# Performance work log

Measured on AMD Instinct MI355X. Metric: run time of the kernel, lower is better.

Reference implementation:

```python
import jax, jax.numpy as jnp
import numpy as np

B, N, DIM = 8, 1024, 1024
H, DH = 16, 64           # heads, dim_head; inner_dim = H*DH = 1024
SCALE = DH ** -0.5


def setup_inputs() -> dict:
    key = jax.random.key(0)
    k_x, k_qkv, k_out, k_b = jax.random.split(key, 4)
    inner = H * DH
    x = jax.random.normal(k_x, (B, N, DIM), dtype=jnp.float32)
    # nn.Linear(dim, inner*3, bias=False): y = x @ W_qkv
    W_qkv = jax.random.normal(k_qkv, (DIM, 3 * inner), dtype=jnp.float32) * (DIM ** -0.5)
    # nn.Linear(inner, dim) with bias (project_out is True since heads!=1)
    W_out = jax.random.normal(k_out, (inner, DIM), dtype=jnp.float32) * (inner ** -0.5)
    b_out = jax.random.normal(k_b, (DIM,), dtype=jnp.float32) * 0.01
    return {"x": x, "W_qkv": W_qkv, "W_out": W_out, "b_out": b_out}


def reference(x, W_qkv, W_out, b_out):
    # 'trans' branch of Attention.forward (dropout p=0 -> identity)
    qkv = x @ W_qkv                                   # [b, n, 3*inner]
    q, k, v = jnp.split(qkv, 3, axis=-1)              # each [b, n, inner]
    def to_heads(t):
        b, n, _ = t.shape
        return t.reshape(b, n, H, DH).transpose(0, 2, 1, 3)  # [b, h, n, d]
    q, k, v = to_heads(q), to_heads(k), to_heads(v)
    dots = jnp.einsum('bhid,bhjd->bhij', q, k) * SCALE  # [b, h, n, n]
    attn = jax.nn.softmax(dots, axis=-1)
    out = jnp.einsum('bhij,bhjd->bhid', attn, v)        # [b, h, n, d]
    # original sets attn = out (b h n d) before merging heads
    attn_ret = out
    out_m = out.transpose(0, 2, 1, 3).reshape(B, N, H * DH)  # [b, n, inner]
    proj = out_m @ W_out + b_out                        # [b, n, dim]
    return (proj, attn_ret)
```

## Files before the change

kernel.cpp:

```cpp
#include <hip/hip_runtime.h>
#include <hip/hip_bf16.h>
#include <math.h>

typedef __bf16 bf16_t;
typedef __bf16 bf16x8 __attribute__((ext_vector_type(8)));
typedef __bf16 bf16x4 __attribute__((ext_vector_type(4)));
typedef float f32x4 __attribute__((ext_vector_type(4)));

#define MFMA16(a, b, c) __builtin_amdgcn_mfma_f32_16x16x32_bf16((a), (b), (c), 0, 0, 0)

#define AS3(p) ((__attribute__((address_space(3))) void*)(p))
#define AS1(p) ((const __attribute__((address_space(1))) void*)(p))

#define B_ 8
#define N_ 1024
#define DIM_ 1024
#define H_ 16
#define DH_ 64

#define QSCALE 0.18033688011112042f
#define SM_SHIFT 12.0f

__global__ __launch_bounds__(256) void k_convert(const float* __restrict__ in,
                                                 bf16_t* __restrict__ out) {
    size_t idx = (size_t)blockIdx.x * 256 + threadIdx.x;
    f32x4 v = *(const f32x4*)(in + idx * 4);
    bf16x4 o;
    o[0] = (bf16_t)v[0]; o[1] = (bf16_t)v[1]; o[2] = (bf16_t)v[2]; o[3] = (bf16_t)v[3];
    *(bf16x4*)(out + idx * 4) = o;
}

__global__ __launch_bounds__(256) void k_transpose(const float* __restrict__ in,
                                                   bf16_t* __restrict__ out,
                                                   int R, int C) {
    __shared__ float tile[32][33];
    int c0 = blockIdx.x * 32, r0 = blockIdx.y * 32;
    int tx = threadIdx.x, ty = threadIdx.y;
#pragma unroll
    for (int i = 0; i < 4; ++i)
        tile[ty + 8 * i][tx] = in[(size_t)(r0 + ty + 8 * i) * C + (c0 + tx)];
    __syncthreads();
#pragma unroll
    for (int i = 0; i < 4; ++i)
        out[(size_t)(c0 + ty + 8 * i) * R + (r0 + tx)] = (bf16_t)tile[tx][ty + 8 * i];
}

__global__ __launch_bounds__(256, 2) void k_gemm_qkv(const bf16_t* __restrict__ A,
                                                     const bf16_t* __restrict__ Bt,
                                                     bf16_t* __restrict__ qb,
                                                     bf16_t* __restrict__ kbuf,
                                                     bf16_t* __restrict__ vtb) {
    __shared__ __align__(16) bf16_t As[256 * 64];
    __shared__ __align__(16) bf16_t Bs[128 * 64];
    int tid = threadIdx.x;
    int lane = tid & 63, wave = tid >> 6;
    int quad = lane >> 4, l16 = lane & 15;
    int m0 = blockIdx.y * 256, c0 = blockIdx.x * 128;
    int wm = (wave & 1) * 128, wn = (wave >> 1) * 64;

    const f32x4 vzero = {0.f, 0.f, 0.f, 0.f};
    f32x4 acc[8][4];
#pragma unroll
    for (int i = 0; i < 8; ++i)
#pragma unroll
        for (int j = 0; j < 4; ++j) acc[i][j] = vzero;

    for (int k0 = 0; k0 < 1024; k0 += 64) {
#pragma unroll
        for (int i = 0; i < 8; ++i) {
            int cid = tid + 256 * i;
            int row = cid >> 3;
            int g = (cid & 7) ^ (row & 7);
            __builtin_amdgcn_global_load_lds(
                AS1(A + (size_t)(m0 + row) * 1024 + k0 + g * 8), AS3(As + cid * 8), 16, 0, 0);
        }
#pragma unroll
        for (int i = 0; i < 4; ++i) {
            int cid = tid + 256 * i;
            int row = cid >> 3;
            int g = (cid & 7) ^ (row & 7);
            __builtin_amdgcn_global_load_lds(
                AS1(Bt + (size_t)(c0 + row) * 1024 + k0 + g * 8), AS3(Bs + cid * 8), 16, 0, 0);
        }
        __syncthreads();
#pragma unroll
        for (int c = 0; c < 2; ++c) {
            int s = (4 * c + quad) ^ (l16 & 7);
            bf16x8 bfr[4];
#pragma unroll
            for (int j = 0; j < 4; ++j)
                bfr[j] = *(const bf16x8*)(Bs + (wn + 16 * j + l16) * 64 + s * 8);
#pragma unroll
            for (int i = 0; i < 8; ++i) {
                bf16x8 af = *(const bf16x8*)(As + (wm + 16 * i + l16) * 64 + s * 8);
#pragma unroll
                for (int j = 0; j < 4; ++j)
                    acc[i][j] = MFMA16(af, bfr[j], acc[i][j]);
            }
        }
        __syncthreads();
    }

    int tsel = c0 >> 10;
#pragma unroll
    for (int i = 0; i < 8; ++i) {
#pragma unroll
        for (int r = 0; r < 4; ++r) {
            int m = m0 + wm + 16 * i + quad * 4 + r;
            int b = m >> 10, n = m & 1023;
#pragma unroll
            for (int j = 0; j < 4; ++j) {
                int cc = c0 + wn + 16 * j + l16;
                int ic = cc & 1023;
                int h = ic >> 6, d = ic & 63;
                float val = acc[i][j][r];
                if (tsel == 0)
                    qb[(((size_t)b * H_ + h) * N_ + n) * DH_ + d] = (bf16_t)(val * QSCALE);
                else if (tsel == 1)
                    kbuf[(((size_t)b * H_ + h) * N_ + n) * DH_ + d] = (bf16_t)val;
                else
                    vtb[(((size_t)b * H_ + h) * DH_ + d) * N_ + n] = (bf16_t)val;
            }
        }
    }
}

__global__ __launch_bounds__(256, 2) void k_attn(const bf16_t* __restrict__ q,
                                                 const bf16_t* __restrict__ k,
                                                 const bf16_t* __restrict__ vt,
                                                 float* __restrict__ oattn,
                                                 bf16_t* __restrict__ outm) {
    __shared__ __align__(16) bf16_t KV[2 * 64 * 72];
    __shared__ __align__(16) bf16_t Ps[4 * 4 * 16 * 72];
    bf16_t* Ks = KV;
    bf16_t* Vs = KV + 64 * 72;
    int tid = threadIdx.x;
    int lane = tid & 63, wave = tid >> 6;
    int quad = lane >> 4, l16 = lane & 15;
    int qt = blockIdx.x & 3;
    int bh = blockIdx.x >> 2;
    int b = bh >> 4, h = bh & 15;

    const bf16_t* qp = q + ((size_t)bh * N_ + qt * 256 + wave * 64) * DH_;
    bf16x8 qa[4][2];
#pragma unroll
    for (int g = 0; g < 4; ++g)
#pragma unroll
        for (int c = 0; c < 2; ++c)
            qa[g][c] = *(const bf16x8*)(qp + (size_t)(g * 16 + l16) * DH_ + c * 32 + quad * 8);

    const bf16_t* kp = k + (size_t)bh * N_ * DH_;
    const bf16_t* vp = vt + (size_t)bh * DH_ * N_;
    bf16_t* Pw = Ps + wave * (4 * 16 * 72);

    const f32x4 vzero = {0.f, 0.f, 0.f, 0.f};
    f32x4 o[4][4];
#pragma unroll
    for (int g = 0; g < 4; ++g)
#pragma unroll
        for (int t = 0; t < 4; ++t) o[g][t] = vzero;
    float lsum[4] = {0.f, 0.f, 0.f, 0.f};

    for (int kb = 0; kb < 16; ++kb) {
#pragma unroll
        for (int i = 0; i < 2; ++i) {
            int cid = tid + 256 * i;
            int row = cid >> 3, ch = (cid & 7) * 8;
            *(bf16x8*)(Ks + row * 72 + ch) =
                *(const bf16x8*)(kp + (size_t)(kb * 64 + row) * DH_ + ch);
            *(bf16x8*)(Vs + row * 72 + ch) =
                *(const bf16x8*)(vp + (size_t)row * N_ + kb * 64 + ch);
        }
        __syncthreads();

        f32x4 st[4][4];
#pragma unroll
        for (int jt = 0; jt < 4; ++jt) {
#pragma unroll
            for (int g = 0; g < 4; ++g) st[g][jt] = vzero;
#pragma unroll
            for (int c = 0; c < 2; ++c) {
                bf16x8 kf = *(const bf16x8*)(Ks + (16 * jt + l16) * 72 + c * 32 + quad * 8);
#pragma unroll
                for (int g = 0; g < 4; ++g)
                    st[g][jt] = MFMA16(kf, qa[g][c], st[g][jt]);
            }
        }

#pragma unroll
        for (int g = 0; g < 4; ++g) {
            float ps = 0.f;
#pragma unroll
            for (int jt = 0; jt < 4; ++jt) {
                bf16x4 pk;
#pragma unroll
                for (int r = 0; r < 4; ++r) {
                    float p = __builtin_amdgcn_exp2f(st[g][jt][r] - SM_SHIFT);
                    ps += p;
                    pk[r] = (bf16_t)p;
                }
                *(bf16x4*)(Pw + g * (16 * 72) + l16 * 72 + jt * 16 + quad * 4) = pk;
            }
            lsum[g] += ps;
        }

        bf16x8 pf[4][2];
#pragma unroll
        for (int g = 0; g < 4; ++g)
#pragma unroll
            for (int c = 0; c < 2; ++c)
                pf[g][c] = *(const bf16x8*)(Pw + g * (16 * 72) + l16 * 72 + c * 32 + quad * 8);
#pragma unroll
        for (int t = 0; t < 4; ++t)
#pragma unroll
            for (int c = 0; c < 2; ++c) {
                bf16x8 vf = *(const bf16x8*)(Vs + (16 * t + l16) * 72 + c * 32 + quad * 8);
#pragma unroll
                for (int g = 0; g < 4; ++g)
                    o[g][t] = MFMA16(vf, pf[g][c], o[g][t]);
            }
        __syncthreads();
    }

#pragma unroll
    for (int g = 0; g < 4; ++g) {
        lsum[g] += __shfl_xor(lsum[g], 16);
        lsum[g] += __shfl_xor(lsum[g], 32);
    }

    float* Ot = (float*)KV + wave * 16 * 68;
#pragma unroll
    for (int g = 0; g < 4; ++g) {
        float inv = 1.f / lsum[g];
#pragma unroll
        for (int t = 0; t < 4; ++t) {
            f32x4 v4;
#pragma unroll
            for (int r = 0; r < 4; ++r) v4[r] = o[g][t][r] * inv;
            *(f32x4*)(Ot + l16 * 68 + t * 16 + quad * 4) = v4;
        }
        int row = lane >> 2, cl = lane & 3;
        int n = qt * 256 + wave * 64 + g * 16 + row;
        const float* orow = Ot + row * 68 + cl * 16;
        float* gout = oattn + ((size_t)bh * N_ + n) * DH_ + cl * 16;
        bf16_t* gm = outm + ((size_t)b * N_ + n) * DIM_ + h * DH_ + cl * 16;
#pragma unroll
        for (int s = 0; s < 4; ++s) {
            f32x4 v = *(const f32x4*)(orow + s * 4);
            *(f32x4*)(gout + s * 4) = v;
            bf16x4 vb;
#pragma unroll
            for (int r = 0; r < 4; ++r) vb[r] = (bf16_t)v[r];
            *(bf16x4*)(gm + s * 4) = vb;
        }
    }
}

__global__ __launch_bounds__(256, 2) void k_gemm_proj(const bf16_t* __restrict__ A,
                                                      const bf16_t* __restrict__ Bt,
                                                      const float* __restrict__ bias,
                                                      float* __restrict__ out) {
    __shared__ __align__(16) bf16_t As[256 * 64];
    __shared__ __align__(16) bf16_t Bs[128 * 64];
    int tid = threadIdx.x;
    int lane = tid & 63, wave = tid >> 6;
    int quad = lane >> 4, l16 = lane & 15;
    int m0 = blockIdx.y * 256, c0 = blockIdx.x * 128;
    int wm = (wave & 1) * 128, wn = (wave >> 1) * 64;

    const f32x4 vzero = {0.f, 0.f, 0.f, 0.f};
    f32x4 acc[8][4];
#pragma unroll
    for (int i = 0; i < 8; ++i)
#pragma unroll
        for (int j = 0; j < 4; ++j) acc[i][j] = vzero;

    for (int k0 = 0; k0 < 1024; k0 += 64) {
#pragma unroll
        for (int i = 0; i < 8; ++i) {
            int cid = tid + 256 * i;
            int row = cid >> 3;
            int g = (cid & 7) ^ (row & 7);
            __builtin_amdgcn_global_load_lds(
                AS1(A + (size_t)(m0 + row) * 1024 + k0 + g * 8), AS3(As + cid * 8), 16, 0, 0);
        }
#pragma unroll
        for (int i = 0; i < 4; ++i) {
            int cid = tid + 256 * i;
            int row = cid >> 3;
            int g = (cid & 7) ^ (row & 7);
            __builtin_amdgcn_global_load_lds(
                AS1(Bt + (size_t)(c0 + row) * 1024 + k0 + g * 8), AS3(Bs + cid * 8), 16, 0, 0);
        }
        __syncthreads();
#pragma unroll
        for (int c = 0; c < 2; ++c) {
            int s = (4 * c + quad) ^ (l16 & 7);
            bf16x8 bfr[4];
#pragma unroll
            for (int j = 0; j < 4; ++j)
                bfr[j] = *(const bf16x8*)(Bs + (wn + 16 * j + l16) * 64 + s * 8);
#pragma unroll
            for (int i = 0; i < 8; ++i) {
                bf16x8 af = *(const bf16x8*)(As + (wm + 16 * i + l16) * 64 + s * 8);
#pragma unroll
                for (int j = 0; j < 4; ++j)
                    acc[i][j] = MFMA16(af, bfr[j], acc[i][j]);
            }
        }
        __syncthreads();
    }

#pragma unroll
    for (int i = 0; i < 8; ++i) {
#pragma unroll
        for (int r = 0; r < 4; ++r) {
            int m = m0 + wm + 16 * i + quad * 4 + r;
#pragma unroll
            for (int j = 0; j < 4; ++j) {
                int cc = c0 + wn + 16 * j + l16;
                out[(size_t)m * DIM_ + cc] = acc[i][j][r] + bias[cc];
            }
        }
    }
}

extern "C" void kernel_launch(void* const* d_in, const int* in_sizes, int n_in,
                              void* d_out, int out_size, void* d_ws, size_t ws_size,
                              hipStream_t stream) {
    const float* x    = (const float*)d_in[0];
    const float* Wqkv = (const float*)d_in[1];
    const float* Wout = (const float*)d_in[2];
    const float* bout = (const float*)d_in[3];

    float* proj  = (float*)d_out;
    float* oattn = proj + (size_t)B_ * N_ * DIM_;

    char* ws = (char*)d_ws;
    const size_t MB = 1024 * 1024;
    bf16_t* xb    = (bf16_t*)(ws);
    bf16_t* wqkvt = (bf16_t*)(ws + 16 * MB);
    bf16_t* woutt = (bf16_t*)(ws + 22 * MB);
    bf16_t* qb    = (bf16_t*)(ws + 24 * MB);
    bf16_t* kbuf  = (bf16_t*)(ws + 40 * MB);
    bf16_t* vtb   = (bf16_t*)(ws + 56 * MB);
    bf16_t* outm  = (bf16_t*)(ws + 72 * MB);

    k_convert<<<8192, 256, 0, stream>>>(x, xb);
    k_transpose<<<dim3(96, 32), dim3(32, 8), 0, stream>>>(Wqkv, wqkvt, 1024, 3072);
    k_transpose<<<dim3(32, 32), dim3(32, 8), 0, stream>>>(Wout, woutt, 1024, 1024);
    k_gemm_qkv<<<dim3(24, 32), 256, 0, stream>>>(xb, wqkvt, qb, kbuf, vtb);
    k_attn<<<512, 256, 0, stream>>>(qb, kbuf, vtb, oattn, outm);
    k_gemm_proj<<<dim3(8, 32), 256, 0, stream>>>(outm, woutt, bout, proj);
}
```

Measured before the change: 286.6 us.

## Merge weight transposes, widen convert, async LDS loads in attention, smaller proj tiles

```diff
diff --git a/kernel.cpp b/kernel.cpp
--- a/kernel.cpp
+++ b/kernel.cpp
@@ -23,18 +23,28 @@
 
 __global__ __launch_bounds__(256) void k_convert(const float* __restrict__ in,
                                                  bf16_t* __restrict__ out) {
-    size_t idx = (size_t)blockIdx.x * 256 + threadIdx.x;
-    f32x4 v = *(const f32x4*)(in + idx * 4);
-    bf16x4 o;
-    o[0] = (bf16_t)v[0]; o[1] = (bf16_t)v[1]; o[2] = (bf16_t)v[2]; o[3] = (bf16_t)v[3];
-    *(bf16x4*)(out + idx * 4) = o;
-}
-
-__global__ __launch_bounds__(256) void k_transpose(const float* __restrict__ in,
-                                                   bf16_t* __restrict__ out,
-                                                   int R, int C) {
+    size_t idx = ((size_t)blockIdx.x * 256 + threadIdx.x) * 8;
+    f32x4 a = *(const f32x4*)(in + idx);
+    f32x4 b = *(const f32x4*)(in + idx + 4);
+    bf16x8 o;
+    o[0] = (bf16_t)a[0]; o[1] = (bf16_t)a[1]; o[2] = (bf16_t)a[2]; o[3] = (bf16_t)a[3];
+    o[4] = (bf16_t)b[0]; o[5] = (bf16_t)b[1]; o[6] = (bf16_t)b[2]; o[7] = (bf16_t)b[3];
+    *(bf16x8*)(out + idx) = o;
+}
+
+__global__ __launch_bounds__(256) void k_prep_w(const float* __restrict__ Wqkv,
+                                                bf16_t* __restrict__ wqkvt,
+                                                const float* __restrict__ Wout,
+                                                bf16_t* __restrict__ woutt) {
     __shared__ float tile[32][33];
-    int c0 = blockIdx.x * 32, r0 = blockIdx.y * 32;
+    int bx = blockIdx.x;
+    const float* in;
+    bf16_t* out;
+    int C, cb;
+    if (bx < 96) { in = Wqkv; out = wqkvt; C = 3072; cb = bx; }
+    else         { in = Wout; out = woutt; C = 1024; cb = bx - 96; }
+    const int R = 1024;
+    int c0 = cb * 32, r0 = blockIdx.y * 32;
     int tx = threadIdx.x, ty = threadIdx.y;
 #pragma unroll
     for (int i = 0; i < 4; ++i)
@@ -130,10 +140,9 @@
                                                  const bf16_t* __restrict__ vt,
                                                  float* __restrict__ oattn,
                                                  bf16_t* __restrict__ outm) {
-    __shared__ __align__(16) bf16_t KV[2 * 64 * 72];
+    __shared__ __align__(16) bf16_t Ks[64 * 64];
+    __shared__ __align__(16) bf16_t Vs[64 * 64];
     __shared__ __align__(16) bf16_t Ps[4 * 4 * 16 * 72];
-    bf16_t* Ks = KV;
-    bf16_t* Vs = KV + 64 * 72;
     int tid = threadIdx.x;
     int lane = tid & 63, wave = tid >> 6;
     int quad = lane >> 4, l16 = lane & 15;
@@ -165,11 +174,12 @@
 #pragma unroll
         for (int i = 0; i < 2; ++i) {
             int cid = tid + 256 * i;
-            int row = cid >> 3, ch = (cid & 7) * 8;
-            *(bf16x8*)(Ks + row * 72 + ch) =
-                *(const bf16x8*)(kp + (size_t)(kb * 64 + row) * DH_ + ch);
-            *(bf16x8*)(Vs + row * 72 + ch) =
-                *(const bf16x8*)(vp + (size_t)row * N_ + kb * 64 + ch);
+            int row = cid >> 3;
+            int g = (cid & 7) ^ (row & 7);
+            __builtin_amdgcn_global_load_lds(
+                AS1(kp + (size_t)(kb * 64 + row) * DH_ + g * 8), AS3(Ks + cid * 8), 16, 0, 0);
+            __builtin_amdgcn_global_load_lds(
+                AS1(vp + (size_t)row * N_ + kb * 64 + g * 8), AS3(Vs + cid * 8), 16, 0, 0);
         }
         __syncthreads();
 
@@ -180,7 +190,8 @@
             for (int g = 0; g < 4; ++g) st[g][jt] = vzero;
 #pragma unroll
             for (int c = 0; c < 2; ++c) {
-                bf16x8 kf = *(const bf16x8*)(Ks + (16 * jt + l16) * 72 + c * 32 + quad * 8);
+                int s = (4 * c + quad) ^ (l16 & 7);
+                bf16x8 kf = *(const bf16x8*)(Ks + (16 * jt + l16) * 64 + s * 8);
 #pragma unroll
                 for (int g = 0; g < 4; ++g)
                     st[g][jt] = MFMA16(kf, qa[g][c], st[g][jt]);
@@ -214,7 +225,8 @@
         for (int t = 0; t < 4; ++t)
 #pragma unroll
             for (int c = 0; c < 2; ++c) {
-                bf16x8 vf = *(const bf16x8*)(Vs + (16 * t + l16) * 72 + c * 32 + quad * 8);
+                int s = (4 * c + quad) ^ (l16 & 7);
+                bf16x8 vf = *(const bf16x8*)(Vs + (16 * t + l16) * 64 + s * 8);
 #pragma unroll
                 for (int g = 0; g < 4; ++g)
                     o[g][t] = MFMA16(vf, pf[g][c], o[g][t]);
@@ -228,7 +240,7 @@
         lsum[g] += __shfl_xor(lsum[g], 32);
     }
 
-    float* Ot = (float*)KV + wave * 16 * 68;
+    float* Ot = (float*)Ps + wave * 16 * 68;
 #pragma unroll
     for (int g = 0; g < 4; ++g) {
         float inv = 1.f / lsum[g];
@@ -256,40 +268,34 @@
     }
 }
 
-__global__ __launch_bounds__(256, 2) void k_gemm_proj(const bf16_t* __restrict__ A,
-                                                      const bf16_t* __restrict__ Bt,
-                                                      const float* __restrict__ bias,
-                                                      float* __restrict__ out) {
-    __shared__ __align__(16) bf16_t As[256 * 64];
+__global__ __launch_bounds__(256) void k_gemm_proj(const bf16_t* __restrict__ A,
+                                                   const bf16_t* __restrict__ Bt,
+                                                   const float* __restrict__ bias,
+                                                   float* __restrict__ out) {
+    __shared__ __align__(16) bf16_t As[128 * 64];
     __shared__ __align__(16) bf16_t Bs[128 * 64];
     int tid = threadIdx.x;
     int lane = tid & 63, wave = tid >> 6;
     int quad = lane >> 4, l16 = lane & 15;
-    int m0 = blockIdx.y * 256, c0 = blockIdx.x * 128;
-    int wm = (wave & 1) * 128, wn = (wave >> 1) * 64;
+    int m0 = blockIdx.y * 128, c0 = blockIdx.x * 128;
+    int wm = (wave & 1) * 64, wn = (wave >> 1) * 64;
 
     const f32x4 vzero = {0.f, 0.f, 0.f, 0.f};
-    f32x4 acc[8][4];
-#pragma unroll
-    for (int i = 0; i < 8; ++i)
+    f32x4 acc[4][4];
+#pragma unroll
+    for (int i = 0; i < 4; ++i)
 #pragma unroll
         for (int j = 0; j < 4; ++j) acc[i][j] = vzero;
 
     for (int k0 = 0; k0 < 1024; k0 += 64) {
-#pragma unroll
-        for (int i = 0; i < 8; ++i) {
-            int cid = tid + 256 * i;
-            int row = cid >> 3;
-            int g = (cid & 7) ^ (row & 7);
-            __builtin_amdgcn_global_load_lds(
-                AS1(A + (size_t)(m0 + row) * 1024 + k0 + g * 8), AS3(As + cid * 8), 16, 0, 0);
-        }
 #pragma unroll
         for (int i = 0; i < 4; ++i) {
             int cid = tid + 256 * i;
             int row = cid >> 3;
             int g = (cid & 7) ^ (row & 7);
             __builtin_amdgcn_global_load_lds(
+                AS1(A + (size_t)(m0 + row) * 1024 + k0 + g * 8), AS3(As + cid * 8), 16, 0, 0);
+            __builtin_amdgcn_global_load_lds(
                 AS1(Bt + (size_t)(c0 + row) * 1024 + k0 + g * 8), AS3(Bs + cid * 8), 16, 0, 0);
         }
         __syncthreads();
@@ -301,7 +307,7 @@
             for (int j = 0; j < 4; ++j)
                 bfr[j] = *(const bf16x8*)(Bs + (wn + 16 * j + l16) * 64 + s * 8);
 #pragma unroll
-            for (int i = 0; i < 8; ++i) {
+            for (int i = 0; i < 4; ++i) {
                 bf16x8 af = *(const bf16x8*)(As + (wm + 16 * i + l16) * 64 + s * 8);
 #pragma unroll
                 for (int j = 0; j < 4; ++j)
@@ -312,7 +318,7 @@
     }
 
 #pragma unroll
-    for (int i = 0; i < 8; ++i) {
+    for (int i = 0; i < 4; ++i) {
 #pragma unroll
         for (int r = 0; r < 4; ++r) {
             int m = m0 + wm + 16 * i + quad * 4 + r;
@@ -346,10 +352,9 @@
     bf16_t* vtb   = (bf16_t*)(ws + 56 * MB);
     bf16_t* outm  = (bf16_t*)(ws + 72 * MB);
 
-    k_convert<<<8192, 256, 0, stream>>>(x, xb);
-    k_transpose<<<dim3(96, 32), dim3(32, 8), 0, stream>>>(Wqkv, wqkvt, 1024, 3072);
-    k_transpose<<<dim3(32, 32), dim3(32, 8), 0, stream>>>(Wout, woutt, 1024, 1024);
+    k_convert<<<4096, 256, 0, stream>>>(x, xb);
+    k_prep_w<<<dim3(128, 32), dim3(32, 8), 0, stream>>>(Wqkv, wqkvt, Wout, woutt);
     k_gemm_qkv<<<dim3(24, 32), 256, 0, stream>>>(xb, wqkvt, qb, kbuf, vtb);
     k_attn<<<512, 256, 0, stream>>>(qb, kbuf, vtb, oattn, outm);
-    k_gemm_proj<<<dim3(8, 32), 256, 0, stream>>>(outm, woutt, bout, proj);
-}
+    k_gemm_proj<<<dim3(8, 64), 256, 0, stream>>>(outm, woutt, bout, proj);
+}
```

Result: faster. 279.6 us (-2.4%).
